# Kernel optimization log

Measured on AMD Instinct MI355X. Metric: run time of the kernel, lower is better.

The kernel has to match this reference:

```python
import jax, jax.numpy as jnp
import numpy as np
from jax import lax

ALPHA = 0.95
THRESH = 1.0
DN = ('NCDHW', 'OIDHW', 'NCDHW')  # (batch, chan, T, H, W)


def lif(x):
    # x: [B, C, T, H, W]. y[t] = (1-a)*y_reset[t-1] + x[t]; s = (y>=th); y *= (1-s)
    xt = jnp.moveaxis(x, 2, 0)  # [T, B, C, H, W]

    def step(y, x_t):
        y = (1.0 - ALPHA) * y + x_t
        s = (y >= THRESH).astype(x.dtype)
        return y * (1.0 - s), s

    _, s = lax.scan(step, jnp.zeros_like(xt[0]), xt)
    return jnp.moveaxis(s, 0, 2)  # back to [B, C, T, H, W]


def delta_encode(x):
    # temporal difference along T (axis 2), zero-padded at t=0
    d = x[:, :, 1:] - x[:, :, :-1]
    return jnp.concatenate([jnp.zeros_like(x[:, :, :1]), d], axis=2)


def setup_inputs() -> dict:
    key = jax.random.key(0)
    ks = jax.random.split(key, 7)
    B, H, W, T = 2, 64, 64, 350
    return {
        'x': jax.random.uniform(ks[0], (B, 2, H, W, T), dtype=jnp.float32),
        'conv1_w': jax.random.normal(ks[1], (8, 2, 5, 5, 1), dtype=jnp.float32) * 0.1,
        'conv1_b': jax.random.normal(ks[2], (8,), dtype=jnp.float32) * 0.1,
        'deconv_w': jax.random.normal(ks[3], (2, 8, 2, 2, 1), dtype=jnp.float32) * 0.1,
        'deconv_b': jax.random.normal(ks[4], (2,), dtype=jnp.float32) * 0.1,
        'conv2_w': jax.random.normal(ks[5], (2, 2), dtype=jnp.float32) * 0.1,
        'conv2_b': jax.random.normal(ks[6], (2,), dtype=jnp.float32) * 0.1,
    }


def reference(x, conv1_w, conv1_b, deconv_w, deconv_b, conv2_w, conv2_b):
    # x: [B, 2, H, W, T] -> [B, 2, T, H, W]
    h = jnp.transpose(x, (0, 1, 4, 2, 3))
    # conv1: kernel (5,5,1) over (T,H,W), padding (2,2,0)
    h = lax.conv_general_dilated(h, conv1_w, (1, 1, 1),
                                 [(2, 2), (2, 2), (0, 0)],
                                 dimension_numbers=DN)
    h = jax.nn.relu(h + conv1_b[None, :, None, None, None])
    h = lif(h)
    h = delta_encode(h)
    # deconv: kernel (2,2,1), stride (2,2,1) -> upsamples T and H by 2
    h = lax.conv_transpose(h, deconv_w, (2, 2, 1), 'VALID',
                           dimension_numbers=DN)
    h = h + deconv_b[None, :, None, None, None]
    # dropout3d(0.1) is identity in eval mode
    h = jax.nn.relu(h)
    # conv2: 1x1x1 conv == channel-mixing matmul
    h = jnp.einsum('oc,bcthw->bothw', conv2_w, h) + conv2_b[None, :, None, None, None]
    h = lif(h)
    # [B, C, T', H', W'] -> [B, C, H', W', T']
    return jnp.transpose(h, (0, 1, 3, 4, 2))
```

## Files before the change

kernel.cpp:

```cpp
#include <hip/hip_runtime.h>

constexpr int B  = 2,  CIN = 2,  H = 64, W = 64, T = 350;
constexpr int C1 = 8;
constexpr int TO = 700, HO = 128, WO = 64;
constexpr int HW = H * W;

#define DEC 0.05000000074505806f

__global__ void __launch_bounds__(256) transpose_kernel(
    const float* __restrict__ x, float* __restrict__ xT) {
  __shared__ float tile[64][65];
  int bid   = blockIdx.x;
  int tTile = bid % 6;
  int slice = bid / 6;
  int h  = slice % H;
  int bc = slice / H;
  int t0 = tTile * 64;
  int tx = threadIdx.x & 63;
  int tz = threadIdx.x >> 6;

  const float* src = x + ((long)bc * H + h) * (long)(W * T);
#pragma unroll
  for (int i = 0; i < 16; ++i) {
    int w = tz * 16 + i;
    int t = t0 + tx;
    tile[w][tx] = (t < T) ? src[(long)w * T + t] : 0.0f;
  }
  __syncthreads();
  float* dst = xT + ((long)bc * T) * HW + h * 64;
#pragma unroll
  for (int i = 0; i < 16; ++i) {
    int tl = tz * 16 + i;
    int t  = t0 + tl;
    if (t < T) dst[(long)t * HW + tx] = tile[tx][tl];
  }
}

__device__ __forceinline__ void gload_lds16(const float* g, float* l) {
  __builtin_amdgcn_global_load_lds(
      (const __attribute__((address_space(1))) unsigned int*)g,
      (__attribute__((address_space(3))) unsigned int*)l, 16, 0, 0);
}

__global__ void __launch_bounds__(512) convlif_kernel(
    const float* __restrict__ xT, const float* __restrict__ w1,
    const float* __restrict__ b1, signed char* __restrict__ d8) {
  __shared__ float bufA[80 * 64];
  __shared__ float bufB[80 * 64];
  __shared__ float dump[16 * 64];
  __shared__ __align__(16) unsigned char st[8][512];
  const int tid = threadIdx.x;
  const int bid = blockIdx.x;
  const int chunk = bid & 7;
  const int rest  = bid >> 3;
  const int h = rest & 63;
  const int b = rest >> 6;
  const int w  = tid & 63;
  const int co = __builtin_amdgcn_readfirstlane(tid >> 6);

  const int tstore = chunk * 48;
  const int ts     = chunk ? tstore - 16 : 0;
  const int te     = tstore + 48 < T ? tstore + 48 : T;
  const int nsup   = (te - ts + 7) / 8;

  float wt[2][5][5];
  float win[2][5][4];
#pragma unroll
  for (int ci = 0; ci < 2; ++ci)
#pragma unroll
    for (int dh = 0; dh < 5; ++dh) {
      int hh = h + dh - 2;
      bool hv = (hh >= 0) && (hh < H);
      int hc = hh < 0 ? 0 : (hh > H - 1 ? H - 1 : hh);
#pragma unroll
      for (int dt = 0; dt < 5; ++dt)
        wt[ci][dt][dh] = hv ? w1[((co * 2 + ci) * 5 + dt) * 5 + dh] : 0.0f;
      const float* bp = xT + ((long)((b * 2 + ci) * T)) * HW + hc * 64 + w;
      win[ci][dh][2] = (ts >= 2) ? bp[(long)(ts - 2) * HW] : 0.0f;
      win[ci][dh][3] = (ts >= 1) ? bp[(long)(ts - 1) * HW] : 0.0f;
      win[ci][dh][0] = bp[(long)(ts + 0) * HW];
      win[ci][dh][1] = bp[(long)(ts + 1) * HW];
    }
  float bias = b1[co];

  int cdesc[3];
#pragma unroll
  for (int i = 0; i < 3; ++i) {
    int r = (tid >> 4) + 32 * i;
    if (r > 79) r = 79;
    int j   = r / 10;
    int rem = r - j * 10;
    int ci  = rem / 5;
    int dh  = rem - ci * 5;
    int hh = h + dh - 2;
    int hc = hh < 0 ? 0 : (hh > H - 1 ? H - 1 : hh);
    cdesc[i] = (((b * 2 + ci) * T) * HW + hc * 64 + (tid & 15) * 4) | (j << 27);
  }
  const int dro0 = (0 * 32 + co * 4) * 64;
  const int dro1 = (1 * 32 + co * 4) * 64;
  const int dro2 = (co < 4) ? (2 * 32 + co * 4) * 64 : ((co - 4) * 4) * 64;
  float* const pad = &dump[0];

  {
    int tau0 = ts + 2 + (cdesc[0] >> 27); if (tau0 > T - 1) tau0 = T - 1;
    int tau1 = ts + 2 + (cdesc[1] >> 27); if (tau1 > T - 1) tau1 = T - 1;
    int tau2 = ts + 2 + (cdesc[2] >> 27); if (tau2 > T - 1) tau2 = T - 1;
    gload_lds16(xT + (long)(cdesc[0] & 0x07ffffff) + (long)tau0 * HW, bufA + dro0);
    gload_lds16(xT + (long)(cdesc[1] & 0x07ffffff) + (long)tau1 * HW, bufA + dro1);
    gload_lds16(xT + (long)(cdesc[2] & 0x07ffffff) + (long)tau2 * HW,
                (co < 4 ? bufA : pad) + dro2);
  }

  asm volatile("s_waitcnt vmcnt(0)" ::: "memory");
  __builtin_amdgcn_s_barrier();
  asm volatile("" ::: "memory");

  signed char* const d8row = d8 + ((long)(b * T)) * (HW * C1) + h * 512;
  const int fl_u  = tid >> 5;
  const int fl_cb = (tid & 31) * 16;
  const int stw   = w * 8 + co;

  float y = 0.0f, sprev = 0.0f;
  for (int k = 0; k < nsup; ++k) {
    asm volatile("s_waitcnt lgkmcnt(0)" ::: "memory");
    __builtin_amdgcn_s_barrier();
    asm volatile("" ::: "memory");

    if (k + 1 < nsup) {
      int bs = ts + 2 + 8 * (k + 1);
      float* nb = ((k + 1) & 1) ? bufB : bufA;
      int tau0 = bs + (cdesc[0] >> 27); if (tau0 > T - 1) tau0 = T - 1;
      int tau1 = bs + (cdesc[1] >> 27); if (tau1 > T - 1) tau1 = T - 1;
      int tau2 = bs + (cdesc[2] >> 27); if (tau2 > T - 1) tau2 = T - 1;
      gload_lds16(xT + (long)(cdesc[0] & 0x07ffffff) + (long)tau0 * HW, nb + dro0);
      gload_lds16(xT + (long)(cdesc[1] & 0x07ffffff) + (long)tau1 * HW, nb + dro1);
      gload_lds16(xT + (long)(cdesc[2] & 0x07ffffff) + (long)tau2 * HW,
                  (co < 4 ? nb : pad) + dro2);
      asm volatile("s_waitcnt vmcnt(3)" ::: "memory");
    } else {
      asm volatile("s_waitcnt vmcnt(0)" ::: "memory");
    }

    if (k > 0 && tid < 256) {
      int t = ts + 8 * (k - 1) + fl_u;
      if (t >= tstore && t < te) {
        uint4 v = *reinterpret_cast<const uint4*>(&st[fl_u][fl_cb]);
        *reinterpret_cast<uint4*>(d8row + (long)t * (HW * C1) + fl_cb) = v;
      }
    }

    asm volatile("s_waitcnt lgkmcnt(0)" ::: "memory");
    __builtin_amdgcn_s_barrier();
    asm volatile("" ::: "memory");

    float* lb = (k & 1) ? bufB : bufA;
    {
      int bufstart = ts + 2 + 8 * k;
      int rz0 = (T - bufstart) * 10;
      if (rz0 < 80) {
        if (rz0 < 0) rz0 = 0;
        for (int r = rz0 + co; r < 80; r += 8) lb[r * 64 + w] = 0.0f;
        asm volatile("s_waitcnt lgkmcnt(0)" ::: "memory");
        __builtin_amdgcn_s_barrier();
        asm volatile("" ::: "memory");
      }
    }

    const int t0s = ts + 8 * k;
#pragma unroll
    for (int u = 0; u < 8; ++u) {
      int t = t0s + u;
      float fr[2][5];
#pragma unroll
      for (int ci = 0; ci < 2; ++ci)
#pragma unroll
        for (int dh = 0; dh < 5; ++dh)
          fr[ci][dh] = lb[(u * 10 + ci * 5 + dh) * 64 + w];

      float ac0 = 0.f, ac1 = 0.f, ac2 = 0.f, ac3 = 0.f;
#pragma unroll
      for (int ci = 0; ci < 2; ++ci)
#pragma unroll
        for (int dt = 0; dt < 5; ++dt)
#pragma unroll
          for (int dh = 0; dh < 5; ++dh) {
            const int q = (ci * 25 + dt * 5 + dh) & 3;
            float tap = (dt < 4) ? win[ci][dh][(u + 2 + dt) & 3] : fr[ci][dh];
            float p = tap * wt[ci][dt][dh];
            if (q == 0) ac0 += p;
            else if (q == 1) ac1 += p;
            else if (q == 2) ac2 += p;
            else ac3 += p;
          }
      float a = ((ac0 + ac1) + (ac2 + ac3)) + bias;
      a = fmaxf(a, 0.0f);
      y = fmaf(DEC, y, a);
      float s = (y >= 1.0f) ? 1.0f : 0.0f;
      float dlt = (t == 0) ? 0.0f : (s - sprev);
      st[u][stw] = (unsigned char)(signed char)dlt;
      sprev = s;
      y = (s != 0.0f) ? 0.0f : y;
#pragma unroll
      for (int ci = 0; ci < 2; ++ci)
#pragma unroll
        for (int dh = 0; dh < 5; ++dh)
          win[ci][dh][(u + 2) & 3] = fr[ci][dh];
    }
  }

  asm volatile("s_waitcnt lgkmcnt(0)" ::: "memory");
  __builtin_amdgcn_s_barrier();
  asm volatile("" ::: "memory");
  if (tid < 256) {
    int t = ts + 8 * (nsup - 1) + fl_u;
    if (t >= tstore && t < te) {
      uint4 v = *reinterpret_cast<const uint4*>(&st[fl_u][fl_cb]);
      *reinterpret_cast<uint4*>(d8row + (long)t * (HW * C1) + fl_cb) = v;
    }
  }
}

__global__ void __launch_bounds__(64) stage2_kernel(
    const signed char* __restrict__ d8, const float* __restrict__ dw,
    const float* __restrict__ db, const float* __restrict__ cw,
    const float* __restrict__ cb, float* __restrict__ out) {
  __shared__ float SB[2][64][17];
  int bid   = blockIdx.x;
  int chunk = bid % 25;
  int rest  = bid / 25;
  int hp = rest & 127;
  int b  = rest >> 7;
  int wp = threadIdx.x;

  int h  = hp >> 1;
  int kh = 1 - (hp & 1);

  float dwk0[2][8], dwk1[2][8];
#pragma unroll
  for (int c = 0; c < 2; ++c)
#pragma unroll
    for (int ci = 0; ci < 8; ++ci) {
      dwk0[c][ci] = dw[((c * 8 + ci) * 2 + 0) * 2 + kh];
      dwk1[c][ci] = dw[((c * 8 + ci) * 2 + 1) * 2 + kh];
    }
  float db0 = db[0], db1 = db[1];
  float cw00 = cw[0], cw01 = cw[1], cw10 = cw[2], cw11 = cw[3];
  float cb0 = cb[0], cb1 = cb[1];

  int t0 = chunk * 28;
  int t1 = t0 + 28;
  int tw = (t0 - 16 > 0) ? t0 - 16 : 0;

  const signed char* dbase = d8 + (((long)b * T) * HW + h * 64 + wp) * C1;
  const long tstride = (long)HW * C1;
  float* outb = out + ((long)b * 2 * HO) * (long)(WO * TO);

  float y0 = 0.0f, y1 = 0.0f;
  uint2 dc = *reinterpret_cast<const uint2*>(dbase + (long)(tw >> 1) * tstride);
  for (int tp = tw; tp < t1; tp += 2) {
    int tn = (tp + 2 < t1) ? ((tp + 2) >> 1) : ((t1 - 1) >> 1);
    uint2 dn = *reinterpret_cast<const uint2*>(dbase + (long)tn * tstride);

    float dv[8];
#pragma unroll
    for (int ci = 0; ci < 4; ++ci) {
      dv[ci]     = (float)(signed char)((dc.x >> (8 * ci)) & 0xff);
      dv[ci + 4] = (float)(signed char)((dc.y >> (8 * ci)) & 0xff);
    }

#pragma unroll
    for (int par = 0; par < 2; ++par) {
      int tpp = tp + par;
      float v0 = db0, v1 = db1;
      if (par == 0) {
#pragma unroll
        for (int ci = 0; ci < 8; ++ci) {
          v0 = fmaf(dv[ci], dwk1[0][ci], v0);
          v1 = fmaf(dv[ci], dwk1[1][ci], v1);
        }
      } else {
#pragma unroll
        for (int ci = 0; ci < 8; ++ci) {
          v0 = fmaf(dv[ci], dwk0[0][ci], v0);
          v1 = fmaf(dv[ci], dwk0[1][ci], v1);
        }
      }
      v0 = fmaxf(v0, 0.0f);
      v1 = fmaxf(v1, 0.0f);
      float u0 = fmaf(cw00, v0, fmaf(cw01, v1, cb0));
      float u1 = fmaf(cw10, v0, fmaf(cw11, v1, cb1));
      y0 = fmaf(DEC, y0, u0);
      y1 = fmaf(DEC, y1, u1);
      float s0 = (y0 >= 1.0f) ? 1.0f : 0.0f;
      float s1 = (y1 >= 1.0f) ? 1.0f : 0.0f;
      y0 = (s0 != 0.0f) ? 0.0f : y0;
      y1 = (s1 != 0.0f) ? 0.0f : y1;

      if (tpp >= t0) {
        int k = (tpp - t0) & 15;
        SB[0][wp][k] = s0;
        SB[1][wp][k] = s1;
        if (par == 1 && (k == 15 || tpp == t1 - 1)) {
          __syncthreads();
          int Kc  = k + 1;
          int t0f = tpp - k;
#pragma unroll
          for (int o = 0; o < 2; ++o) {
            float* ob = outb + ((long)(o * HO + hp)) * (long)(WO * TO);
#pragma unroll
            for (int i = 0; i < 4; ++i) {
              int idx = (i << 6) + wp;
              int r   = idx >> 2;
              int c   = (idx & 3) << 2;
              if (c < Kc) {
                float4 vv;
                vv.x = SB[o][r][c + 0];
                vv.y = SB[o][r][c + 1];
                vv.z = SB[o][r][c + 2];
                vv.w = SB[o][r][c + 3];
                *reinterpret_cast<float4*>(ob + (long)r * TO + (t0f + c)) = vv;
              }
            }
          }
          __syncthreads();
        }
      }
    }
    dc = dn;
  }
}

extern "C" void kernel_launch(void* const* d_in, const int* in_sizes, int n_in,
                              void* d_out, int out_size, void* d_ws, size_t ws_size,
                              hipStream_t stream) {
  const float* x  = (const float*)d_in[0];
  const float* w1 = (const float*)d_in[1];
  const float* b1 = (const float*)d_in[2];
  const float* dw = (const float*)d_in[3];
  const float* db = (const float*)d_in[4];
  const float* cw = (const float*)d_in[5];
  const float* cb = (const float*)d_in[6];
  float* out = (float*)d_out;

  float* xT = (float*)d_ws;
  signed char* d8 = (signed char*)d_ws + (size_t)B * CIN * T * HW * 4;

  transpose_kernel<<<dim3(B * CIN * H * 6), dim3(256), 0, stream>>>(x, xT);
  convlif_kernel<<<dim3(B * H * 8), dim3(512), 0, stream>>>(xT, w1, b1, d8);
  stage2_kernel<<<dim3(B * HO * 25), dim3(64), 0, stream>>>(d8, dw, db, cw, cb, out);
}
```

Before: 122.4 us.

## Split fused conv+LIF into parallel conv kernel and time-chunked LIF kernel

Replaces the fused convolution+LIF kernel with two kernels, used only when the workspace is large enough. The first computes the 5x5 conv over time tiles in parallel and writes the fp32 activations to a new workspace buffer. The second runs the LIF recurrence in independent time chunks, warming each chunk up over the previous 16 steps, then writes the delta-encoded int8 spikes. This breaks the serial time dependency to expose more parallelism, but adds a large fp32 intermediate write and read-back. The warm-up truncation also relies on the 0.05 decay making older state negligible.

```diff
diff --git a/kernel.cpp b/kernel.cpp
--- a/kernel.cpp
+++ b/kernel.cpp
@@ -40,6 +40,173 @@
   __builtin_amdgcn_global_load_lds(
       (const __attribute__((address_space(1))) unsigned int*)g,
       (__attribute__((address_space(3))) unsigned int*)l, 16, 0, 0);
+}
+
+__global__ void __launch_bounds__(512) convpar_kernel(
+    const float* __restrict__ xT, const float* __restrict__ w1,
+    const float* __restrict__ b1, float* __restrict__ A) {
+  __shared__ float lb[160 * 64];
+  const int tid  = threadIdx.x;
+  const int bid  = blockIdx.x;
+  const int h    = bid & 63;
+  const int rest = bid >> 6;
+  const int tile = rest % 30;
+  const int b    = rest / 30;
+  const int t0   = tile * 12;
+  const int co   = tid & 7;
+  const int w    = tid >> 3;
+  const int wid  = tid >> 6;
+
+  float wt[2][5][5];
+#pragma unroll
+  for (int ci = 0; ci < 2; ++ci)
+#pragma unroll
+    for (int dh = 0; dh < 5; ++dh) {
+      int hh = h + dh - 2;
+      bool hv = (hh >= 0) && (hh < H);
+#pragma unroll
+      for (int dt = 0; dt < 5; ++dt)
+        wt[ci][dt][dh] = hv ? w1[((co * 2 + ci) * 5 + dt) * 5 + dh] : 0.0f;
+    }
+  float bias = b1[co];
+
+  int cdesc[5];
+#pragma unroll
+  for (int i = 0; i < 5; ++i) {
+    int r   = (tid >> 4) + 32 * i;
+    int j   = r / 10;
+    int rem = r - j * 10;
+    int ci  = rem / 5;
+    int dh  = rem - ci * 5;
+    int hh = h + dh - 2;
+    int hc = hh < 0 ? 0 : (hh > H - 1 ? H - 1 : hh);
+    cdesc[i] = (((b * 2 + ci) * T) * HW + hc * 64 + (tid & 15) * 4) | (j << 27);
+  }
+#pragma unroll
+  for (int i = 0; i < 5; ++i) {
+    int tau = t0 - 2 + (cdesc[i] >> 27);
+    tau = tau < 0 ? 0 : (tau > T - 1 ? T - 1 : tau);
+    gload_lds16(xT + (long)(cdesc[i] & 0x07ffffff) + (long)tau * HW,
+                &lb[(i * 32 + wid * 4) * 64]);
+  }
+  __syncthreads();
+
+  {
+    int rlo = (t0 >= 2) ? 0 : (2 - t0) * 10;
+    int rhiv = (T - t0 + 2) * 10;
+    int rhi = rhiv > 160 ? 160 : rhiv;
+    if (rlo > 0 || rhi < 160) {
+      for (int s = tid; s < rlo * 64; s += 512) lb[s] = 0.0f;
+      for (int s = rhi * 64 + tid; s < 160 * 64; s += 512) lb[s] = 0.0f;
+      __syncthreads();
+    }
+  }
+
+  float win[2][5][4];
+#pragma unroll
+  for (int ci = 0; ci < 2; ++ci)
+#pragma unroll
+    for (int dh = 0; dh < 5; ++dh) {
+      const int cd = ci * 5 + dh;
+      win[ci][dh][2] = lb[(0  + cd) * 64 + w];
+      win[ci][dh][3] = lb[(10 + cd) * 64 + w];
+      win[ci][dh][0] = lb[(20 + cd) * 64 + w];
+      win[ci][dh][1] = lb[(30 + cd) * 64 + w];
+    }
+
+  float* const Abase = A + (((long)(b * T)) * HW + h * 64 + w) * 8 + co;
+#pragma unroll
+  for (int u = 0; u < 12; ++u) {
+    int t = t0 + u;
+    float fr[2][5];
+#pragma unroll
+    for (int ci = 0; ci < 2; ++ci)
+#pragma unroll
+      for (int dh = 0; dh < 5; ++dh)
+        fr[ci][dh] = lb[((u + 4) * 10 + ci * 5 + dh) * 64 + w];
+
+    float ac0 = 0.f, ac1 = 0.f, ac2 = 0.f, ac3 = 0.f;
+#pragma unroll
+    for (int ci = 0; ci < 2; ++ci)
+#pragma unroll
+      for (int dt = 0; dt < 5; ++dt)
+#pragma unroll
+        for (int dh = 0; dh < 5; ++dh) {
+          const int q = (ci * 25 + dt * 5 + dh) & 3;
+          float tap = (dt < 4) ? win[ci][dh][(u + 2 + dt) & 3] : fr[ci][dh];
+          float p = tap * wt[ci][dt][dh];
+          if (q == 0) ac0 += p;
+          else if (q == 1) ac1 += p;
+          else if (q == 2) ac2 += p;
+          else ac3 += p;
+        }
+    float a = ((ac0 + ac1) + (ac2 + ac3)) + bias;
+    a = fmaxf(a, 0.0f);
+    if (t < T) Abase[(long)t * (HW * C1)] = a;
+#pragma unroll
+    for (int ci = 0; ci < 2; ++ci)
+#pragma unroll
+      for (int dh = 0; dh < 5; ++dh)
+        win[ci][dh][(u + 2) & 3] = fr[ci][dh];
+  }
+}
+
+__global__ void __launch_bounds__(256) lif_kernel(
+    const float* __restrict__ A, signed char* __restrict__ d8) {
+  const int tid   = threadIdx.x;
+  const int bid   = blockIdx.x;
+  const int chunk = bid & 7;
+  const int hwh   = (bid >> 3) & 15;
+  const int b     = bid >> 7;
+  const int hw    = hwh * 256 + tid;
+
+  const int t0 = chunk * 44;
+  const int te = (t0 + 44 < T) ? t0 + 44 : T;
+  const int tw = (t0 >= 16) ? t0 - 16 : 0;
+
+  const float4* Ab = reinterpret_cast<const float4*>(
+      A + (((long)(b * T)) * HW + hw) * 8);
+  const long ts4 = (long)HW * 2;
+  signed char* db = d8 + (((long)(b * T)) * HW + hw) * 8;
+  const long tsb = (long)HW * 8;
+
+  float y0=0,y1=0,y2=0,y3=0,y4=0,y5=0,y6=0,y7=0;
+  float p0=0,p1=0,p2=0,p3=0,p4=0,p5=0,p6=0,p7=0;
+
+  float4 a0 = Ab[(long)tw * ts4];
+  float4 a1 = Ab[(long)tw * ts4 + 1];
+  for (int t = tw; t < te; ++t) {
+    int tn = (t + 1 < te) ? t + 1 : t;
+    float4 n0 = Ab[(long)tn * ts4];
+    float4 n1 = Ab[(long)tn * ts4 + 1];
+
+    float s0,s1,s2,s3,s4,s5,s6,s7;
+    y0 = fmaf(DEC, y0, a0.x); s0 = (y0 >= 1.0f) ? 1.0f : 0.0f; y0 = (s0!=0.0f)?0.0f:y0;
+    y1 = fmaf(DEC, y1, a0.y); s1 = (y1 >= 1.0f) ? 1.0f : 0.0f; y1 = (s1!=0.0f)?0.0f:y1;
+    y2 = fmaf(DEC, y2, a0.z); s2 = (y2 >= 1.0f) ? 1.0f : 0.0f; y2 = (s2!=0.0f)?0.0f:y2;
+    y3 = fmaf(DEC, y3, a0.w); s3 = (y3 >= 1.0f) ? 1.0f : 0.0f; y3 = (s3!=0.0f)?0.0f:y3;
+    y4 = fmaf(DEC, y4, a1.x); s4 = (y4 >= 1.0f) ? 1.0f : 0.0f; y4 = (s4!=0.0f)?0.0f:y4;
+    y5 = fmaf(DEC, y5, a1.y); s5 = (y5 >= 1.0f) ? 1.0f : 0.0f; y5 = (s5!=0.0f)?0.0f:y5;
+    y6 = fmaf(DEC, y6, a1.z); s6 = (y6 >= 1.0f) ? 1.0f : 0.0f; y6 = (s6!=0.0f)?0.0f:y6;
+    y7 = fmaf(DEC, y7, a1.w); s7 = (y7 >= 1.0f) ? 1.0f : 0.0f; y7 = (s7!=0.0f)?0.0f:y7;
+
+    if (t >= t0) {
+      unsigned int lo = 0, hi = 0;
+      lo |= ((unsigned int)(int)(s0 - p0) & 0xffu);
+      lo |= ((unsigned int)(int)(s1 - p1) & 0xffu) << 8;
+      lo |= ((unsigned int)(int)(s2 - p2) & 0xffu) << 16;
+      lo |= ((unsigned int)(int)(s3 - p3) & 0xffu) << 24;
+      hi |= ((unsigned int)(int)(s4 - p4) & 0xffu);
+      hi |= ((unsigned int)(int)(s5 - p5) & 0xffu) << 8;
+      hi |= ((unsigned int)(int)(s6 - p6) & 0xffu) << 16;
+      hi |= ((unsigned int)(int)(s7 - p7) & 0xffu) << 24;
+      if (t == 0) { lo = 0u; hi = 0u; }
+      uint2 v; v.x = lo; v.y = hi;
+      *reinterpret_cast<uint2*>(db + (long)t * tsb) = v;
+    }
+    p0=s0; p1=s1; p2=s2; p3=s3; p4=s4; p5=s5; p6=s6; p7=s7;
+    a0 = n0; a1 = n1;
+  }
 }
 
 __global__ void __launch_bounds__(512) convlif_kernel(
@@ -342,10 +509,22 @@
   const float* cb = (const float*)d_in[6];
   float* out = (float*)d_out;
 
+  const size_t xT_b = (size_t)4 * B * CIN * T * HW;
+  const size_t d8_b = (size_t)B * T * HW * C1;
+  const size_t A_b  = (size_t)4 * B * T * HW * C1;
+
   float* xT = (float*)d_ws;
-  signed char* d8 = (signed char*)d_ws + (size_t)B * CIN * T * HW * 4;
+  signed char* d8 = (signed char*)d_ws + xT_b;
 
   transpose_kernel<<<dim3(B * CIN * H * 6), dim3(256), 0, stream>>>(x, xT);
-  convlif_kernel<<<dim3(B * H * 8), dim3(512), 0, stream>>>(xT, w1, b1, d8);
+
+  if (ws_size >= xT_b + d8_b + A_b) {
+    float* A = (float*)((char*)d_ws + xT_b + d8_b);
+    convpar_kernel<<<dim3(B * 30 * H), dim3(512), 0, stream>>>(xT, w1, b1, A);
+    lif_kernel<<<dim3(B * 16 * 8), dim3(256), 0, stream>>>(A, d8);
+  } else {
+    convlif_kernel<<<dim3(B * H * 8), dim3(512), 0, stream>>>(xT, w1, b1, d8);
+  }
+
   stage2_kernel<<<dim3(B * HO * 25), dim3(64), 0, stream>>>(d8, dw, db, cw, cb, out);
 }
```

Result: slower. 159.4 us (+30.2%).
